# Kernel tuning notes

Measured on AMD Instinct MI355X. Metric: run time of the kernel, lower is better.

The kernel has to match this reference:

```python
import jax, jax.numpy as jnp
import numpy as np

N_NODES = 100_000
N_EDGES = 3_200_000
EPS_BN = 1e-5
EPS_NORM = 1e-12


def _sage_conv(x, src, dst, ew, pw, pb, lw, lb, rw, n_nodes):
    # project=True: relu(Linear_in->in) applied to source features
    xp = jax.nn.relu(x @ pw + pb)                       # [N, in]
    msg = xp[src] * ew[:, None]                         # [E, in] gather + weight
    agg = jax.ops.segment_sum(msg, dst, num_segments=n_nodes)      # scatter-sum
    cnt = jax.ops.segment_sum(jnp.ones_like(ew), dst, num_segments=n_nodes)
    mean = agg / jnp.maximum(cnt, 1.0)[:, None]         # scatter-mean
    out = mean @ lw + lb + x @ rw                       # neighbor lin + root lin
    # normalize=True: L2 normalize rows
    nrm = jnp.sqrt(jnp.sum(out * out, axis=-1, keepdims=True))
    return out / jnp.maximum(nrm, EPS_NORM)


def setup_inputs() -> dict:
    key = jax.random.key(0)
    ks = jax.random.split(key, 20)
    d = {}
    d["h"] = jax.random.normal(ks[0], (N_NODES, 5), dtype=jnp.float32)
    d["edge_index"] = jax.random.randint(ks[1], (2, N_EDGES), 0, N_NODES, dtype=jnp.int32)
    d["edge_weight"] = jax.random.uniform(ks[2], (N_EDGES,), dtype=jnp.float32)
    # BatchNorm1d(5) params (conv2_norm in the source is unused in forward)
    d["bn_gamma"] = jnp.ones((5,), jnp.float32)
    d["bn_beta"] = jnp.zeros((5,), jnp.float32)

    def lin(k, fan_in, fan_out):
        return jax.random.normal(k, (fan_in, fan_out), jnp.float32) * (1.0 / np.sqrt(fan_in))

    # conv1: 5 -> 64 ; conv2: 64 -> 64 (fixing source bug) ; conv3: 64 -> 5
    dims = [(5, 64), (64, 64), (64, 5)]
    ki = 3
    for i, (fi, fo) in enumerate(dims, start=1):
        d[f"c{i}_pw"] = lin(ks[ki], fi, fi); ki += 1
        d[f"c{i}_pb"] = jnp.zeros((fi,), jnp.float32)
        d[f"c{i}_lw"] = lin(ks[ki], fi, fo); ki += 1
        d[f"c{i}_lb"] = jnp.zeros((fo,), jnp.float32)
        d[f"c{i}_rw"] = lin(ks[ki], fi, fo); ki += 1
    return d


def reference(h, edge_index, edge_weight, bn_gamma, bn_beta,
              c1_pw, c1_pb, c1_lw, c1_lb, c1_rw,
              c2_pw, c2_pb, c2_lw, c2_lb, c2_rw,
              c3_pw, c3_pb, c3_lw, c3_lb, c3_rw):
    src, dst = edge_index[0], edge_index[1]
    # BatchNorm1d (training-mode batch statistics, biased variance)
    mu = jnp.mean(h, axis=0)
    var = jnp.mean((h - mu) ** 2, axis=0)
    x = (h - mu) * jax.lax.rsqrt(var + EPS_BN) * bn_gamma + bn_beta

    x = jax.nn.relu(_sage_conv(x, src, dst, edge_weight, c1_pw, c1_pb, c1_lw, c1_lb, c1_rw, N_NODES))
    x = jax.nn.relu(_sage_conv(x, src, dst, edge_weight, c2_pw, c2_pb, c2_lw, c2_lb, c2_rw, N_NODES))
    x = _sage_conv(x, src, dst, edge_weight, c3_pw, c3_pb, c3_lw, c3_lb, c3_rw, N_NODES)
    # dropout omitted (deterministic / eval-mode reference)
    return x
```

## Files before the change

### kernel.cpp

```cpp
#include <hip/hip_runtime.h>
#include <hip/hip_bf16.h>

#define N_NODES 100000
#define N_EDGES 3200000
#define BSH 8
#define NB 391

typedef __hip_bfloat16 bf16;

#define RL(v, k) __int_as_float(__builtin_amdgcn_readlane(__float_as_int(v), (k)))

__device__ __forceinline__ float loadF(const void* p, long long i, int isf32) {
    if (isf32) return ((const float*)p)[i];
    unsigned short v = ((const unsigned short*)p)[i];
    union { unsigned u; float f; } c;
    c.u = ((unsigned)v) << 16;
    return c.f;
}

__device__ __forceinline__ unsigned packEdge(int s, float w) {
    bf16 b = __float2bfloat16(w);
    unsigned short bits = *(unsigned short*)&b;
    return ((unsigned)s << 15) | (unsigned)(bits & 0x7FFF);
}
__device__ __forceinline__ int edgeSrc(unsigned u) { return (int)(u >> 15); }
__device__ __forceinline__ float edgeW(unsigned u) {
    union { unsigned x; float f; } c;
    c.x = (u & 0x7FFFu) << 16;
    return c.f;
}

#define W_GAMMA 0
#define W_BETA 8
#define W_C1PW 16
#define W_C1PB 48
#define W_C1LW 56
#define W_C1LB 376
#define W_C1RW 440
#define W_C2PW 760
#define W_C2PB 4856
#define W_C2LW 4920
#define W_C2LB 9016
#define W_C2RW 9080
#define W_C3PW 13176
#define W_C3PB 17272
#define W_C3LW 17336
#define W_C3LB 17656
#define W_C3RW 17664

__global__ void detect_dtype(const void* ew, int* flag) {
    const unsigned short* u = (const unsigned short*)ew;
    int lane = threadIdx.x;
    int big = 0;
    for (int i = lane; i < 1024; i += 64) {
        unsigned short v = u[2 * i];
        int ex = (v >> 7) & 0xFF;
        if (ex >= 128) big++;
    }
#pragma unroll
    for (int o = 32; o; o >>= 1) big += __shfl_xor(big, o, 64);
    if (lane == 0) *flag = (big > 100) ? 1 : 0;
}

__global__ void cvt_weights(const int* flag,
                            const void* p0, const void* p1, const void* p2, const void* p3,
                            const void* p4, const void* p5, const void* p6, const void* p7,
                            const void* p8, const void* p9, const void* p10, const void* p11,
                            const void* p12, const void* p13, const void* p14, const void* p15,
                            const void* p16, float* __restrict__ wts) {
    const void* ptrs[17] = {p0, p1, p2, p3, p4, p5, p6, p7, p8,
                            p9, p10, p11, p12, p13, p14, p15, p16};
    const int sz[17] = {5, 5, 25, 5, 320, 64, 320, 4096, 64,
                        4096, 64, 4096, 4096, 64, 320, 5, 320};
    const int off[17] = {W_GAMMA, W_BETA, W_C1PW, W_C1PB, W_C1LW, W_C1LB, W_C1RW,
                         W_C2PW, W_C2PB, W_C2LW, W_C2LB, W_C2RW,
                         W_C3PW, W_C3PB, W_C3LW, W_C3LB, W_C3RW};
    int t = blockIdx.x;
    int isf32 = *flag;
    for (int i = threadIdx.x; i < sz[t]; i += blockDim.x)
        wts[off[t] + i] = loadF(ptrs[t], i, isf32);
}

__global__ void bn_stats(const void* __restrict__ h, const int* __restrict__ flag,
                         float* __restrict__ stats) {
    int isf32 = *flag;
    float s[5] = {0, 0, 0, 0, 0}, q[5] = {0, 0, 0, 0, 0};
    int tid = blockIdx.x * blockDim.x + threadIdx.x;
    int stride = gridDim.x * blockDim.x;
    for (int i = tid; i < N_NODES; i += stride) {
#pragma unroll
        for (int f = 0; f < 5; f++) {
            float v = loadF(h, i * 5 + f, isf32);
            s[f] += v;
            q[f] += v * v;
        }
    }
#pragma unroll
    for (int f = 0; f < 5; f++) {
#pragma unroll
        for (int o = 32; o; o >>= 1) {
            s[f] += __shfl_xor(s[f], o, 64);
            q[f] += __shfl_xor(q[f], o, 64);
        }
    }
    __shared__ float ls[4][10];
    int wave = threadIdx.x >> 6, lane = threadIdx.x & 63;
    if (lane == 0) {
#pragma unroll
        for (int f = 0; f < 5; f++) { ls[wave][f] = s[f]; ls[wave][5 + f] = q[f]; }
    }
    __syncthreads();
    if (threadIdx.x < 10) {
        float v = ls[0][threadIdx.x] + ls[1][threadIdx.x] + ls[2][threadIdx.x] + ls[3][threadIdx.x];
        int idx = (threadIdx.x < 5) ? threadIdx.x : (threadIdx.x - 5 + 8);
        atomicAdd(&stats[idx], v);
    }
}

__global__ void bn_proj1(const void* __restrict__ h, const int* __restrict__ flag,
                         const float* __restrict__ stats, const float* __restrict__ wts,
                         float* __restrict__ xbn, float* __restrict__ xp1) {
    __shared__ float s_sc[5], s_sb[5];
    if (threadIdx.x < 5) {
        int f = threadIdx.x;
        float mean = stats[f] / (float)N_NODES;
        float var = stats[8 + f] / (float)N_NODES - mean * mean;
        float sc = wts[W_GAMMA + f] * rsqrtf(var + 1e-5f);
        s_sc[f] = sc;
        s_sb[f] = wts[W_BETA + f] - mean * sc;
    }
    __syncthreads();
    int isf32 = *flag;
    int i = blockIdx.x * blockDim.x + threadIdx.x;
    if (i >= N_NODES) return;
    float x[5];
#pragma unroll
    for (int f = 0; f < 5; f++)
        x[f] = loadF(h, i * 5 + f, isf32) * s_sc[f] + s_sb[f];
#pragma unroll
    for (int f = 0; f < 5; f++) xbn[i * 5 + f] = x[f];
#pragma unroll
    for (int j = 0; j < 5; j++) {
        float a = wts[W_C1PB + j];
#pragma unroll
        for (int k = 0; k < 5; k++) a += x[k] * wts[W_C1PW + k * 5 + j];
        xp1[i * 5 + j] = fmaxf(a, 0.f);
    }
}

__global__ void __launch_bounds__(256) bucket_hist(const int* __restrict__ dst,
                                                   int* __restrict__ bucketCnt) {
    __shared__ int hcnt[NB];
    for (int i = threadIdx.x; i < NB; i += 256) hcnt[i] = 0;
    __syncthreads();
    int per = (N_EDGES + gridDim.x - 1) / gridDim.x;
    int s = blockIdx.x * per;
    int e = min(s + per, N_EDGES);
    for (int i = s + threadIdx.x; i < e; i += 256)
        atomicAdd(&hcnt[dst[i] >> BSH], 1);
    __syncthreads();
    for (int i = threadIdx.x; i < NB; i += 256)
        if (hcnt[i]) atomicAdd(&bucketCnt[i], hcnt[i]);
}

__global__ void __launch_bounds__(512) bucket_scan(const int* __restrict__ bucketCnt,
                                                   int* __restrict__ bucketStart,
                                                   int* __restrict__ bucketCursor) {
    int tid = threadIdx.x, lane = tid & 63, w = tid >> 6;
    int v = (tid < NB) ? bucketCnt[tid] : 0;
    int sc = v;
#pragma unroll
    for (int o = 1; o < 64; o <<= 1) {
        int t = __shfl_up(sc, o, 64);
        if (lane >= o) sc += t;
    }
    __shared__ int ws[8];
    if (lane == 63) ws[w] = sc;
    __syncthreads();
    if (w == 0) {
        int wv = (lane < 8) ? ws[lane] : 0;
        int s2 = wv;
#pragma unroll
        for (int o = 1; o < 8; o <<= 1) {
            int t = __shfl_up(s2, o, 64);
            if (lane >= o) s2 += t;
        }
        if (lane < 8) ws[lane] = s2;
    }
    __syncthreads();
    int woff = w ? ws[w - 1] : 0;
    int ex = woff + sc - v;
    if (tid < NB) {
        bucketStart[tid] = ex;
        bucketCursor[tid] = ex;
    }
    if (tid == 0) bucketStart[NB] = N_EDGES;
}

__global__ void __launch_bounds__(256) bucket_stage(const int* __restrict__ src,
                                                    const int* __restrict__ dst,
                                                    const void* __restrict__ ew,
                                                    const int* __restrict__ flag,
                                                    int* __restrict__ bucketCursor,
                                                    uint2* __restrict__ stage) {
    __shared__ int hcnt[NB], cur[NB];
    int isf32 = *flag;
    for (int i = threadIdx.x; i < NB; i += 256) hcnt[i] = 0;
    __syncthreads();
    int per = (N_EDGES + gridDim.x - 1) / gridDim.x;
    int s = blockIdx.x * per;
    int e = min(s + per, N_EDGES);
    for (int i = s + threadIdx.x; i < e; i += 256)
        atomicAdd(&hcnt[dst[i] >> BSH], 1);
    __syncthreads();
    for (int i = threadIdx.x; i < NB; i += 256)
        cur[i] = hcnt[i] ? atomicAdd(&bucketCursor[i], hcnt[i]) : 0;
    __syncthreads();
    for (int i = s + threadIdx.x; i < e; i += 256) {
        int d = dst[i];
        int slot = atomicAdd(&cur[d >> BSH], 1);
        stage[slot] = make_uint2((unsigned)d, packEdge(src[i], loadF(ew, i, isf32)));
    }
}

__global__ void __launch_bounds__(256) bucket_place(const uint2* __restrict__ stage,
                                                    const int* __restrict__ bucketStart,
                                                    int* __restrict__ start,
                                                    unsigned* __restrict__ perm) {
    int b = blockIdx.x, tid = threadIdx.x;
    int base = bucketStart[b];
    int cnt = bucketStart[b + 1] - base;
    int n0 = b << BSH;
    int nn = min(256, N_NODES - n0);
    __shared__ int lcnt[256], loff[256], ws[4];
    lcnt[tid] = 0;
    __syncthreads();
    for (int i = tid; i < cnt; i += 256)
        atomicAdd(&lcnt[stage[base + i].x & 255], 1);
    __syncthreads();
    int lane = tid & 63, w = tid >> 6;
    int v = lcnt[tid];
    int sc = v;
#pragma unroll
    for (int o = 1; o < 64; o <<= 1) {
        int t = __shfl_up(sc, o, 64);
        if (lane >= o) sc += t;
    }
    if (lane == 63) ws[w] = sc;
    __syncthreads();
    int woff = 0;
    for (int k = 0; k < w; k++) woff += ws[k];
    loff[tid] = woff + sc - v;
    __syncthreads();
    if (tid < nn) start[n0 + tid] = base + loff[tid];
    if (b == 0 && tid == 0) start[N_NODES] = N_EDGES;
    lcnt[tid] = 0;
    __syncthreads();
    for (int i = tid; i < cnt; i += 256) {
        uint2 sv = stage[base + i];
        int l = sv.x & 255;
        int p = atomicAdd(&lcnt[l], 1);
        perm[base + loff[l] + p] = sv.y;
    }
}

__global__ void agg5(const float* __restrict__ y, const int* __restrict__ start,
                     const unsigned* __restrict__ perm, float* __restrict__ agg) {
    int n = blockIdx.x * blockDim.x + threadIdx.x;
    if (n >= N_NODES) return;
    int e0 = start[n], e1 = start[n + 1];
    float a[5] = {0, 0, 0, 0, 0};
    int e = e0;
    for (; e + 4 <= e1; e += 4) {
        unsigned p0 = perm[e], p1 = perm[e + 1], p2 = perm[e + 2], p3 = perm[e + 3];
        const float* r0 = y + (size_t)edgeSrc(p0) * 5;
        const float* r1 = y + (size_t)edgeSrc(p1) * 5;
        const float* r2 = y + (size_t)edgeSrc(p2) * 5;
        const float* r3 = y + (size_t)edgeSrc(p3) * 5;
        float v0[5], v1[5], v2[5], v3[5];
#pragma unroll
        for (int f = 0; f < 5; f++) { v0[f] = r0[f]; v1[f] = r1[f]; v2[f] = r2[f]; v3[f] = r3[f]; }
        float w0 = edgeW(p0), w1 = edgeW(p1), w2 = edgeW(p2), w3 = edgeW(p3);
#pragma unroll
        for (int f = 0; f < 5; f++)
            a[f] += v0[f] * w0 + v1[f] * w1 + v2[f] * w2 + v3[f] * w3;
    }
    for (; e < e1; e++) {
        unsigned p = perm[e];
        float w = edgeW(p);
        const float* row = y + (size_t)edgeSrc(p) * 5;
#pragma unroll
        for (int f = 0; f < 5; f++) a[f] += row[f] * w;
    }
    size_t b = (size_t)n * 5;
#pragma unroll
    for (int f = 0; f < 5; f++) agg[b + f] = a[f];
}

__global__ void __launch_bounds__(256) epi1_proj2(const float* __restrict__ agg,
                                                  const int* __restrict__ start,
                                                  const float* __restrict__ xbn,
                                                  const float* __restrict__ wts,
                                                  float* __restrict__ x1,
                                                  bf16* __restrict__ y2) {
    int lane = threadIdx.x & 63;
    int wid = __builtin_amdgcn_readfirstlane((blockIdx.x * blockDim.x + threadIdx.x) >> 6);
    int nw = (gridDim.x * blockDim.x) >> 6;
    float Wlw[5], Wrw[5];
#pragma unroll
    for (int k = 0; k < 5; k++) {
        Wlw[k] = wts[W_C1LW + k * 64 + lane];
        Wrw[k] = wts[W_C1RW + k * 64 + lane];
    }
    float lb = wts[W_C1LB + lane];
    float W1[64], W2[64];
#pragma unroll
    for (int k = 0; k < 64; k++) W1[k] = wts[W_C2PW + k * 64 + lane];
#pragma unroll
    for (int k = 0; k < 64; k++) W2[k] = wts[W_C2LW + k * 64 + lane];
    float pb = wts[W_C2PB + lane];
    for (int node = wid; node < N_NODES; node += nw) {
        float ic = 1.f / fmaxf((float)(start[node + 1] - start[node]), 1.f);
        float mv = 0.f, xb = 0.f;
        if (lane < 5) {
            mv = agg[node * 5 + lane] * ic;
            xb = xbn[node * 5 + lane];
        }
        float out = lb;
#pragma unroll
        for (int k = 0; k < 5; k++)
            out += RL(mv, k) * Wlw[k] + RL(xb, k) * Wrw[k];
        float ss = out * out;
#pragma unroll
        for (int o = 32; o; o >>= 1) ss += __shfl_xor(ss, o, 64);
        float xv = fmaxf(out / fmaxf(sqrtf(ss), 1e-12f), 0.f);
        x1[(size_t)node * 64 + lane] = xv;
        float a0 = pb, a1 = 0.f, a2 = 0.f, a3 = 0.f;
#pragma unroll
        for (int k = 0; k < 64; k += 4) {
            a0 += RL(xv, k) * W1[k];
            a1 += RL(xv, k + 1) * W1[k + 1];
            a2 += RL(xv, k + 2) * W1[k + 2];
            a3 += RL(xv, k + 3) * W1[k + 3];
        }
        float xp = fmaxf((a0 + a1) + (a2 + a3), 0.f);
        float b0 = 0.f, b1 = 0.f, b2 = 0.f, b3 = 0.f;
#pragma unroll
        for (int k = 0; k < 64; k += 4) {
            b0 += RL(xp, k) * W2[k];
            b1 += RL(xp, k + 1) * W2[k + 1];
            b2 += RL(xp, k + 2) * W2[k + 2];
            b3 += RL(xp, k + 3) * W2[k + 3];
        }
        y2[(size_t)node * 64 + lane] = __float2bfloat16((b0 + b1) + (b2 + b3));
    }
}

__global__ void __launch_bounds__(256) conv2_fused_reg(const bf16* __restrict__ y2,
                                                       const int* __restrict__ start,
                                                       const unsigned* __restrict__ perm,
                                                       const float* __restrict__ x1,
                                                       const float* __restrict__ wts,
                                                       float* __restrict__ x2) {
    int lane = threadIdx.x & 63;
    int wid = __builtin_amdgcn_readfirstlane((blockIdx.x * blockDim.x + threadIdx.x) >> 6);
    int nw = (gridDim.x * blockDim.x) >> 6;
    float W[64];
#pragma unroll
    for (int k = 0; k < 64; k++) W[k] = wts[W_C2RW + k * 64 + lane];
    float lb = wts[W_C2LB + lane];
    for (int node = wid; node < N_NODES; node += nw) {
        int e0 = start[node], e1 = start[node + 1];
        float acc = 0.f;
        int e = e0;
        for (; e + 8 <= e1; e += 8) {
            unsigned p[8];
#pragma unroll
            for (int u = 0; u < 8; u++) p[u] = perm[e + u];
            float v[8];
#pragma unroll
            for (int u = 0; u < 8; u++)
                v[u] = __bfloat162float(y2[(size_t)edgeSrc(p[u]) * 64 + lane]);
#pragma unroll
            for (int u = 0; u < 8; u++) acc += v[u] * edgeW(p[u]);
        }
        for (; e < e1; e++) {
            unsigned p = perm[e];
            acc += __bfloat162float(y2[(size_t)edgeSrc(p) * 64 + lane]) * edgeW(p);
        }
        float ic = 1.f / fmaxf((float)(e1 - e0), 1.f);
        float xv = x1[(size_t)node * 64 + lane];
        float o0 = acc * ic + lb, o1 = 0.f, o2 = 0.f, o3 = 0.f;
#pragma unroll
        for (int k = 0; k < 64; k += 4) {
            o0 += RL(xv, k) * W[k];
            o1 += RL(xv, k + 1) * W[k + 1];
            o2 += RL(xv, k + 2) * W[k + 2];
            o3 += RL(xv, k + 3) * W[k + 3];
        }
        float out = (o0 + o1) + (o2 + o3);
        float ss = out * out;
#pragma unroll
        for (int o = 32; o; o >>= 1) ss += __shfl_xor(ss, o, 64);
        float v = out / fmaxf(sqrtf(ss), 1e-12f);
        x2[(size_t)node * 64 + lane] = fmaxf(v, 0.f);
    }
}

__global__ void __launch_bounds__(256) proj3_reg(const float* __restrict__ x2,
                                                 const float* __restrict__ wts,
                                                 float* __restrict__ y3) {
    int lane = threadIdx.x & 63;
    int wid = __builtin_amdgcn_readfirstlane((blockIdx.x * blockDim.x + threadIdx.x) >> 6);
    int nw = (gridDim.x * blockDim.x) >> 6;
    float W1[64], Wl[5];
#pragma unroll
    for (int k = 0; k < 64; k++) W1[k] = wts[W_C3PW + k * 64 + lane];
#pragma unroll
    for (int j = 0; j < 5; j++) Wl[j] = wts[W_C3LW + lane * 5 + j];
    float pb = wts[W_C3PB + lane];
    for (int node = wid; node < N_NODES; node += nw) {
        float xv = x2[(size_t)node * 64 + lane];
        float a0 = pb, a1 = 0.f, a2 = 0.f, a3 = 0.f;
#pragma unroll
        for (int k = 0; k < 64; k += 4) {
            a0 += RL(xv, k) * W1[k];
            a1 += RL(xv, k + 1) * W1[k + 1];
            a2 += RL(xv, k + 2) * W1[k + 2];
            a3 += RL(xv, k + 3) * W1[k + 3];
        }
        float xp = fmaxf((a0 + a1) + (a2 + a3), 0.f);
#pragma unroll
        for (int j = 0; j < 5; j++) {
            float p = xp * Wl[j];
#pragma unroll
            for (int o = 32; o; o >>= 1) p += __shfl_xor(p, o, 64);
            if (lane == j) y3[node * 5 + j] = p;
        }
    }
}

__global__ void __launch_bounds__(256) epilogue3(const float* __restrict__ agg,
                                                 const int* __restrict__ start,
                                                 const float* __restrict__ x2,
                                                 const float* __restrict__ wts,
                                                 const int* __restrict__ flag,
                                                 void* __restrict__ outp) {
    __shared__ float s_rw[64 * 5];
    for (int t = threadIdx.x; t < 320; t += 256) s_rw[t] = wts[W_C3RW + t];
    __syncthreads();
    int isf32 = *flag;
    int wave = threadIdx.x >> 6, lane = threadIdx.x & 63;
    int node = blockIdx.x * 4 + wave;
    if (node >= N_NODES) return;
    float ic = 1.f / fmaxf((float)(start[node + 1] - start[node]), 1.f);
    float xv = x2[(size_t)node * 64 + lane];
    float r[5];
#pragma unroll
    for (int j = 0; j < 5; j++) {
        float p = xv * s_rw[lane * 5 + j];
#pragma unroll
        for (int o = 32; o; o >>= 1) p += __shfl_xor(p, o, 64);
        r[j] = p + agg[node * 5 + j] * ic + wts[W_C3LB + j];
    }
    float ss = 0.f;
#pragma unroll
    for (int j = 0; j < 5; j++) ss += r[j] * r[j];
    float inv = 1.f / fmaxf(sqrtf(ss), 1e-12f);
#pragma unroll
    for (int j = 0; j < 5; j++) {
        if (lane == j) {
            float v = r[j] * inv;
            if (isf32) ((float*)outp)[node * 5 + j] = v;
            else ((bf16*)outp)[node * 5 + j] = __float2bfloat16(v);
        }
    }
}

extern "C" void kernel_launch(void* const* d_in, const int* in_sizes, int n_in,
                              void* d_out, int out_size, void* d_ws, size_t ws_size,
                              hipStream_t stream) {
    const void* h = d_in[0];
    const int* ei = (const int*)d_in[1];
    const int* src = ei;
    const int* dst = ei + N_EDGES;
    const void* ew = d_in[2];

    float* W = (float*)d_ws;
    int* flag = (int*)W;
    float* stats = W + 16;
    float* wts = W + 64;
    float* xbn = W + 20480;
    float* xp1 = xbn + N_NODES * 5;
    int* startp = (int*)(xp1 + N_NODES * 5);
    int* bucketCnt = startp + N_NODES + 64;
    int* bucketStart = bucketCnt + NB + 1;
    int* bucketCursor = bucketStart + NB + 1;
    unsigned* perm = (unsigned*)(bucketCursor + NB + 62);
    float* x1 = (float*)(perm + N_EDGES);
    uint2* stage = (uint2*)x1;
    bf16* y2 = (bf16*)(x1 + (size_t)N_NODES * 64);
    float* aggbuf = (float*)(y2 + (size_t)N_NODES * 64);
    float* x2 = x1;
    float* y3 = xp1;

    detect_dtype<<<1, 64, 0, stream>>>(ew, flag);
    cvt_weights<<<17, 256, 0, stream>>>(flag,
        d_in[3], d_in[4],
        d_in[5], d_in[6], d_in[7], d_in[8], d_in[9],
        d_in[10], d_in[11], d_in[12], d_in[13], d_in[14],
        d_in[15], d_in[16], d_in[17], d_in[18], d_in[19],
        wts);

    hipMemsetAsync(stats, 0, 32 * sizeof(float), stream);
    hipMemsetAsync(bucketCnt, 0, NB * sizeof(int), stream);

    bn_stats<<<200, 256, 0, stream>>>(h, flag, stats);
    bn_proj1<<<(N_NODES + 255) / 256, 256, 0, stream>>>(h, flag, stats, wts, xbn, xp1);

    bucket_hist<<<256, 256, 0, stream>>>(dst, bucketCnt);
    bucket_scan<<<1, 512, 0, stream>>>(bucketCnt, bucketStart, bucketCursor);
    bucket_stage<<<256, 256, 0, stream>>>(src, dst, ew, flag, bucketCursor, stage);
    bucket_place<<<NB, 256, 0, stream>>>(stage, bucketStart, startp, perm);

    agg5<<<(N_NODES + 255) / 256, 256, 0, stream>>>(xp1, startp, perm, aggbuf);
    epi1_proj2<<<1024, 256, 0, stream>>>(aggbuf, startp, xbn, wts, x1, y2);

    conv2_fused_reg<<<2048, 256, 0, stream>>>(y2, startp, perm, x1, wts, x2);

    proj3_reg<<<1024, 256, 0, stream>>>(x2, wts, y3);
    agg5<<<(N_NODES + 255) / 256, 256, 0, stream>>>(y3, startp, perm, aggbuf);
    epilogue3<<<N_NODES / 4, 256, 0, stream>>>(aggbuf, startp, x2, wts, flag, d_out);
}
```

Measured before the change: 581.1 us.

## Fuse 5-dim aggregation into conv1 and conv3 epilogues, deepen conv2 unroll

The separate agg5 kernels for conv1 and conv3 are removed. Each wave now gathers a node's edges lane-parallel, reduces the 5 sums with cross-lane shuffles, and feeds them straight into the epilogue, which drops a kernel launch and the intermediate agg buffer round-trip each time. conv2's edge loop is unrolled from 8 to 16 with a 4-wide tail, and its grid is doubled. The trade-off is a wave-per-node layout for 5-wide aggregation, which leaves lanes idle for low-degree nodes, plus added shuffle-reduction cost and higher register pressure in conv2.

Measured after the change: 574.1 us. Within noise of the previous version (-1.2%).

```diff
diff --git a/kernel.cpp b/kernel.cpp
--- a/kernel.cpp
+++ b/kernel.cpp
@@ -264,45 +264,13 @@
     }
 }
 
-__global__ void agg5(const float* __restrict__ y, const int* __restrict__ start,
-                     const unsigned* __restrict__ perm, float* __restrict__ agg) {
-    int n = blockIdx.x * blockDim.x + threadIdx.x;
-    if (n >= N_NODES) return;
-    int e0 = start[n], e1 = start[n + 1];
-    float a[5] = {0, 0, 0, 0, 0};
-    int e = e0;
-    for (; e + 4 <= e1; e += 4) {
-        unsigned p0 = perm[e], p1 = perm[e + 1], p2 = perm[e + 2], p3 = perm[e + 3];
-        const float* r0 = y + (size_t)edgeSrc(p0) * 5;
-        const float* r1 = y + (size_t)edgeSrc(p1) * 5;
-        const float* r2 = y + (size_t)edgeSrc(p2) * 5;
-        const float* r3 = y + (size_t)edgeSrc(p3) * 5;
-        float v0[5], v1[5], v2[5], v3[5];
-#pragma unroll
-        for (int f = 0; f < 5; f++) { v0[f] = r0[f]; v1[f] = r1[f]; v2[f] = r2[f]; v3[f] = r3[f]; }
-        float w0 = edgeW(p0), w1 = edgeW(p1), w2 = edgeW(p2), w3 = edgeW(p3);
-#pragma unroll
-        for (int f = 0; f < 5; f++)
-            a[f] += v0[f] * w0 + v1[f] * w1 + v2[f] * w2 + v3[f] * w3;
-    }
-    for (; e < e1; e++) {
-        unsigned p = perm[e];
-        float w = edgeW(p);
-        const float* row = y + (size_t)edgeSrc(p) * 5;
-#pragma unroll
-        for (int f = 0; f < 5; f++) a[f] += row[f] * w;
-    }
-    size_t b = (size_t)n * 5;
-#pragma unroll
-    for (int f = 0; f < 5; f++) agg[b + f] = a[f];
-}
-
-__global__ void __launch_bounds__(256) epi1_proj2(const float* __restrict__ agg,
-                                                  const int* __restrict__ start,
-                                                  const float* __restrict__ xbn,
-                                                  const float* __restrict__ wts,
-                                                  float* __restrict__ x1,
-                                                  bf16* __restrict__ y2) {
+__global__ void __launch_bounds__(256) conv1_fused(const float* __restrict__ xp1,
+                                                   const float* __restrict__ xbn,
+                                                   const int* __restrict__ start,
+                                                   const unsigned* __restrict__ perm,
+                                                   const float* __restrict__ wts,
+                                                   float* __restrict__ x1,
+                                                   bf16* __restrict__ y2) {
     int lane = threadIdx.x & 63;
     int wid = __builtin_amdgcn_readfirstlane((blockIdx.x * blockDim.x + threadIdx.x) >> 6);
     int nw = (gridDim.x * blockDim.x) >> 6;
@@ -320,16 +288,32 @@
     for (int k = 0; k < 64; k++) W2[k] = wts[W_C2LW + k * 64 + lane];
     float pb = wts[W_C2PB + lane];
     for (int node = wid; node < N_NODES; node += nw) {
-        float ic = 1.f / fmaxf((float)(start[node + 1] - start[node]), 1.f);
-        float mv = 0.f, xb = 0.f;
-        if (lane < 5) {
-            mv = agg[node * 5 + lane] * ic;
-            xb = xbn[node * 5 + lane];
-        }
-        float out = lb;
-#pragma unroll
-        for (int k = 0; k < 5; k++)
-            out += RL(mv, k) * Wlw[k] + RL(xb, k) * Wrw[k];
+        int e0 = start[node], e1 = start[node + 1];
+        float s0 = 0, s1 = 0, s2 = 0, s3 = 0, s4 = 0;
+        for (int eb = e0; eb < e1; eb += 64) {
+            int e = eb + lane;
+            if (e < e1) {
+                unsigned p = perm[e];
+                float w = edgeW(p);
+                const float* row = xp1 + (size_t)edgeSrc(p) * 5;
+                s0 += row[0] * w; s1 += row[1] * w; s2 += row[2] * w;
+                s3 += row[3] * w; s4 += row[4] * w;
+            }
+        }
+#pragma unroll
+        for (int o = 32; o; o >>= 1) {
+            s0 += __shfl_xor(s0, o, 64);
+            s1 += __shfl_xor(s1, o, 64);
+            s2 += __shfl_xor(s2, o, 64);
+            s3 += __shfl_xor(s3, o, 64);
+            s4 += __shfl_xor(s4, o, 64);
+        }
+        float ic = 1.f / fmaxf((float)(e1 - e0), 1.f);
+        float xb = (lane < 5) ? xbn[node * 5 + lane] : 0.f;
+        float out = lb + s0 * ic * Wlw[0] + s1 * ic * Wlw[1] + s2 * ic * Wlw[2] +
+                    s3 * ic * Wlw[3] + s4 * ic * Wlw[4];
+#pragma unroll
+        for (int k = 0; k < 5; k++) out += RL(xb, k) * Wrw[k];
         float ss = out * out;
 #pragma unroll
         for (int o = 32; o; o >>= 1) ss += __shfl_xor(ss, o, 64);
@@ -373,16 +357,27 @@
         int e0 = start[node], e1 = start[node + 1];
         float acc = 0.f;
         int e = e0;
-        for (; e + 8 <= e1; e += 8) {
-            unsigned p[8];
-#pragma unroll
-            for (int u = 0; u < 8; u++) p[u] = perm[e + u];
-            float v[8];
-#pragma unroll
-            for (int u = 0; u < 8; u++)
+        for (; e + 16 <= e1; e += 16) {
+            unsigned p[16];
+#pragma unroll
+            for (int u = 0; u < 16; u++) p[u] = perm[e + u];
+            float v[16];
+#pragma unroll
+            for (int u = 0; u < 16; u++)
                 v[u] = __bfloat162float(y2[(size_t)edgeSrc(p[u]) * 64 + lane]);
 #pragma unroll
-            for (int u = 0; u < 8; u++) acc += v[u] * edgeW(p[u]);
+            for (int u = 0; u < 16; u++) acc += v[u] * edgeW(p[u]);
+        }
+        for (; e + 4 <= e1; e += 4) {
+            unsigned p[4];
+#pragma unroll
+            for (int u = 0; u < 4; u++) p[u] = perm[e + u];
+            float v[4];
+#pragma unroll
+            for (int u = 0; u < 4; u++)
+                v[u] = __bfloat162float(y2[(size_t)edgeSrc(p[u]) * 64 + lane]);
+#pragma unroll
+            for (int u = 0; u < 4; u++) acc += v[u] * edgeW(p[u]);
         }
         for (; e < e1; e++) {
             unsigned p = perm[e];
@@ -440,39 +435,64 @@
     }
 }
 
-__global__ void __launch_bounds__(256) epilogue3(const float* __restrict__ agg,
-                                                 const int* __restrict__ start,
-                                                 const float* __restrict__ x2,
-                                                 const float* __restrict__ wts,
-                                                 const int* __restrict__ flag,
-                                                 void* __restrict__ outp) {
-    __shared__ float s_rw[64 * 5];
-    for (int t = threadIdx.x; t < 320; t += 256) s_rw[t] = wts[W_C3RW + t];
-    __syncthreads();
+__global__ void __launch_bounds__(256) conv3_fused(const float* __restrict__ y3,
+                                                   const float* __restrict__ x2,
+                                                   const int* __restrict__ start,
+                                                   const unsigned* __restrict__ perm,
+                                                   const float* __restrict__ wts,
+                                                   const int* __restrict__ flag,
+                                                   void* __restrict__ outp) {
+    int lane = threadIdx.x & 63;
+    int wid = __builtin_amdgcn_readfirstlane((blockIdx.x * blockDim.x + threadIdx.x) >> 6);
+    int nw = (gridDim.x * blockDim.x) >> 6;
+    float Wr[5];
+#pragma unroll
+    for (int j = 0; j < 5; j++) Wr[j] = wts[W_C3RW + lane * 5 + j];
+    float lb3[5];
+#pragma unroll
+    for (int j = 0; j < 5; j++) lb3[j] = wts[W_C3LB + j];
     int isf32 = *flag;
-    int wave = threadIdx.x >> 6, lane = threadIdx.x & 63;
-    int node = blockIdx.x * 4 + wave;
-    if (node >= N_NODES) return;
-    float ic = 1.f / fmaxf((float)(start[node + 1] - start[node]), 1.f);
-    float xv = x2[(size_t)node * 64 + lane];
-    float r[5];
-#pragma unroll
-    for (int j = 0; j < 5; j++) {
-        float p = xv * s_rw[lane * 5 + j];
-#pragma unroll
-        for (int o = 32; o; o >>= 1) p += __shfl_xor(p, o, 64);
-        r[j] = p + agg[node * 5 + j] * ic + wts[W_C3LB + j];
-    }
-    float ss = 0.f;
-#pragma unroll
-    for (int j = 0; j < 5; j++) ss += r[j] * r[j];
-    float inv = 1.f / fmaxf(sqrtf(ss), 1e-12f);
-#pragma unroll
-    for (int j = 0; j < 5; j++) {
-        if (lane == j) {
-            float v = r[j] * inv;
-            if (isf32) ((float*)outp)[node * 5 + j] = v;
-            else ((bf16*)outp)[node * 5 + j] = __float2bfloat16(v);
+    for (int node = wid; node < N_NODES; node += nw) {
+        int e0 = start[node], e1 = start[node + 1];
+        float s0 = 0, s1 = 0, s2 = 0, s3 = 0, s4 = 0;
+        for (int eb = e0; eb < e1; eb += 64) {
+            int e = eb + lane;
+            if (e < e1) {
+                unsigned p = perm[e];
+                float w = edgeW(p);
+                const float* row = y3 + (size_t)edgeSrc(p) * 5;
+                s0 += row[0] * w; s1 += row[1] * w; s2 += row[2] * w;
+                s3 += row[3] * w; s4 += row[4] * w;
+            }
+        }
+#pragma unroll
+        for (int o = 32; o; o >>= 1) {
+            s0 += __shfl_xor(s0, o, 64);
+            s1 += __shfl_xor(s1, o, 64);
+            s2 += __shfl_xor(s2, o, 64);
+            s3 += __shfl_xor(s3, o, 64);
+            s4 += __shfl_xor(s4, o, 64);
+        }
+        float ic = 1.f / fmaxf((float)(e1 - e0), 1.f);
+        float xv = x2[(size_t)node * 64 + lane];
+        float m[5] = {s0 * ic, s1 * ic, s2 * ic, s3 * ic, s4 * ic};
+        float r[5], ss = 0.f;
+#pragma unroll
+        for (int j = 0; j < 5; j++) {
+            float p = xv * Wr[j];
+#pragma unroll
+            for (int o = 32; o; o >>= 1) p += __shfl_xor(p, o, 64);
+            r[j] = p + m[j] + lb3[j];
+            ss += r[j] * r[j];
+        }
+        float inv = 1.f / fmaxf(sqrtf(ss), 1e-12f);
+#pragma unroll
+        for (int j = 0; j < 5; j++) {
+            if (lane == j) {
+                float v = r[j] * inv;
+                if (isf32) ((float*)outp)[node * 5 + j] = v;
+                else ((bf16*)outp)[node * 5 + j] = __float2bfloat16(v);
+            }
         }
     }
 }
@@ -500,7 +520,6 @@
     float* x1 = (float*)(perm + N_EDGES);
     uint2* stage = (uint2*)x1;
     bf16* y2 = (bf16*)(x1 + (size_t)N_NODES * 64);
-    float* aggbuf = (float*)(y2 + (size_t)N_NODES * 64);
     float* x2 = x1;
     float* y3 = xp1;
 
@@ -523,12 +542,10 @@
     bucket_stage<<<256, 256, 0, stream>>>(src, dst, ew, flag, bucketCursor, stage);
     bucket_place<<<NB, 256, 0, stream>>>(stage, bucketStart, startp, perm);
 
-    agg5<<<(N_NODES + 255) / 256, 256, 0, stream>>>(xp1, startp, perm, aggbuf);
-    epi1_proj2<<<1024, 256, 0, stream>>>(aggbuf, startp, xbn, wts, x1, y2);
-
-    conv2_fused_reg<<<2048, 256, 0, stream>>>(y2, startp, perm, x1, wts, x2);
+    conv1_fused<<<2048, 256, 0, stream>>>(xp1, xbn, startp, perm, wts, x1, y2);
+
+    conv2_fused_reg<<<4096, 256, 0, stream>>>(y2, startp, perm, x1, wts, x2);
 
     proj3_reg<<<1024, 256, 0, stream>>>(x2, wts, y3);
-    agg5<<<(N_NODES + 255) / 256, 256, 0, stream>>>(y3, startp, perm, aggbuf);
-    epilogue3<<<N_NODES / 4, 256, 0, stream>>>(aggbuf, startp, x2, wts, flag, d_out);
-}
+    conv3_fused<<<2048, 256, 0, stream>>>(y3, x2, startp, perm, wts, flag, d_out);
+}
```
